# Kernel optimization log

Measured on AMD Instinct MI355X. Metric: run time of the kernel, lower is better.

The kernel has to match this reference:

```python
import jax, jax.numpy as jnp
import numpy as np

NU, NI, G, D, HD, OD = 8000, 10000, 4096, 64, 64, 64
ALPHA = 0.8      # self vs neighbor mixing in NodeApplyModule
EPS = 1e-8       # cosine-similarity denominator epsilon
NEG_BIG = -1e38  # replacement for all -inf rows


def setup_inputs() -> dict:
    key = jax.random.key(0)
    ks = jax.random.split(key, 24)
    def lin(k, o, i):
        return (jax.random.normal(k, (o, i), jnp.float32) * 0.02)
    def bias(k, o):
        return (jax.random.normal(k, (o,), jnp.float32) * 0.02)
    inp = {}
    inp["H"] = jax.random.randint(ks[0], (NU + NI, G), 0, 2, jnp.int32)
    inp["feats_weight"] = jax.random.normal(ks[1], (NU + NI, D), jnp.float32) * 0.1
    inp["num_groups"] = G
    # user SelfAttention params
    inp["u_Wq"] = lin(ks[2], HD, D); inp["u_bq"] = bias(ks[3], HD)
    inp["u_Wk"] = lin(ks[4], HD, D); inp["u_bk"] = bias(ks[5], HD)
    inp["u_Wv"] = lin(ks[6], HD, D); inp["u_bv"] = bias(ks[7], HD)
    inp["u_Ws"] = lin(ks[8], 1, NU); inp["u_bs"] = bias(ks[9], 1)
    # item SelfAttention params
    inp["i_Wq"] = lin(ks[10], HD, D); inp["i_bq"] = bias(ks[11], HD)
    inp["i_Wk"] = lin(ks[12], HD, D); inp["i_bk"] = bias(ks[13], HD)
    inp["i_Wv"] = lin(ks[14], HD, D); inp["i_bv"] = bias(ks[15], HD)
    inp["i_Ws"] = lin(ks[16], 1, NI); inp["i_bs"] = bias(ks[17], 1)
    # WeightedGCN NodeApplyModule linear: in_feats = 2*HD -> out_feats = OD
    inp["g_W"] = lin(ks[18], OD, 2 * HD); inp["g_b"] = bias(ks[19], OD)
    return inp


def _self_attention(x, mask, num_groups, Wq, bq, Wk, bk, Wv, bv, Ws, bs):
    # x: [N, D] ; mask: [N, G]
    q = x @ Wq.T + bq            # [N, HD]
    k = x @ Wk.T + bk            # [N, HD]
    v = x @ Wv.T + bv            # [N, HD]
    s = (q @ k.T) @ Ws.T + bs    # [N, 1]  (Linear(num_elem,1) over q@k.T)
    scores = jnp.broadcast_to(s.reshape(1, -1), (num_groups, x.shape[0]))  # [G, N]
    maskT = (mask == 0).T        # [G, N]
    scores = jnp.where(maskT, -jnp.inf, scores)
    all_inf = jnp.all(scores == -jnp.inf, axis=1, keepdims=True)
    scores = jnp.where(all_inf, jnp.float32(NEG_BIG), scores)
    w = jax.nn.softmax(scores, axis=1)   # [G, N]
    return w @ v, w                      # [G, HD], [G, N]


def reference(H, feats_weight, num_groups,
              u_Wq, u_bq, u_Wk, u_bk, u_Wv, u_bv, u_Ws, u_bs,
              i_Wq, i_bq, i_Wk, i_bk, i_Wv, i_bv, i_Ws, i_bs,
              g_W, g_b):
    users_feats = feats_weight[:NU]
    items_feats = feats_weight[NU:]
    users_mask = H[:NU]
    items_mask = H[NU:]

    gf_u, w_u = _self_attention(users_feats, users_mask, num_groups,
                                u_Wq, u_bq, u_Wk, u_bk, u_Wv, u_bv, u_Ws, u_bs)
    gf_i, w_i = _self_attention(items_feats, items_mask, num_groups,
                                i_Wq, i_bq, i_Wk, i_bk, i_Wv, i_bv, i_Ws, i_bs)
    # NaN scrubbing (faithful to torch.where(isnan, 0, .))
    gf_i = jnp.where(jnp.isnan(gf_i), 0.0, gf_i)
    w_i = jnp.where(jnp.isnan(w_i), 0.0, w_i)

    group_weights = jnp.concatenate([w_u, w_i], axis=1)   # [G, NU+NI]
    group_feats = jnp.concatenate([gf_u, gf_i], axis=1)   # [G, 2*HD]

    # similarity graph (cosine similarity of group weight rows)
    wp = group_weights @ group_weights.T                  # [G, G]
    norms = jnp.sqrt(jnp.sum(group_weights * group_weights, axis=1))
    l2 = 1.0 / (norms[:, None] * norms[None, :] + EPS)
    A = wp * l2  # edge weight src->dst at A[src, dst]; zero WP entries contribute 0

    # weighted mean aggregation (DGL msg/reduce: sum(w*h)/sum(w) over in-edges)
    msg = A.T @ group_feats                 # [G, 2*HD]: sum_src A[src,dst]*h[src]
    deg = jnp.sum(A, axis=0)[:, None]       # [G, 1]:   sum_src A[src,dst]
    h_neigh = jnp.where(deg > 0, msg / jnp.where(deg > 0, deg, 1.0), 0.0)

    agg = ALPHA * group_feats + (1.0 - ALPHA) * h_neigh
    out = jax.nn.sigmoid(agg @ g_W.T + g_b)               # [G, OD]
    return out
```

## Files before the change

kernel.cpp:

```cpp
#include <hip/hip_runtime.h>
#include <hip/hip_bf16.h>
#include <cstdint>
#include <cstddef>

#define NU   8000
#define NI   10000
#define NTOT 18000
#define G    4096
#define KP2  18176
#define NSL  284
#define NSL128 142
#define KT8  142
#define UT8  63

typedef __attribute__((ext_vector_type(4))) float f32x4;

__device__ __forceinline__ float bfu(unsigned short u){
  return __uint_as_float(((unsigned)u)<<16);
}
__device__ __forceinline__ unsigned short f2b(float f){
  __hip_bfloat16 h = __float2bfloat16(f);
  return __builtin_bit_cast(unsigned short, h);
}
__device__ __forceinline__ unsigned char f2f8(float v){
  int p = __builtin_amdgcn_cvt_pk_fp8_f32(v, 0.f, 0, false);
  return (unsigned char)(p & 0xff);
}
template<int SEL>
__device__ __forceinline__ float f8tof(unsigned int w){
  return __builtin_amdgcn_cvt_f32_fp8((int)w, SEL);
}
__device__ __forceinline__ void async16(void* lds, const void* g){
  __builtin_amdgcn_global_load_lds((const __attribute__((address_space(1))) unsigned int*)g,
                                   (__attribute__((address_space(3))) unsigned int*)lds, 16, 0, 0);
}
__device__ __forceinline__ int slot2n(int s){
  return (s < 8064) ? (s < 8000 ? s : -1) : (s-64 < NTOT ? s-64 : -1);
}

__global__ __launch_bounds__(256) void k_proj(
    const float* __restrict__ feats,
    const float* uWq, const float* ubq, const float* uWk, const float* ubk,
    const float* uWv, const float* ubv, const float* uWs,
    const float* iWq, const float* ibq, const float* iWk, const float* ibk,
    const float* iWv, const float* ibv, const float* iWs,
    float* __restrict__ q, unsigned short* __restrict__ vrow, float* __restrict__ wsk)
{
  __shared__ unsigned short Wt[6*4096];
  __shared__ float bl[6*64];
  __shared__ float wacc[128];
  const float* mats[6]  = {uWq,uWk,uWv,iWq,iWk,iWv};
  const float* bias6[6] = {ubq,ubk,ubv,ibq,ibk,ibv};
  int t = threadIdx.x;
  for (int m=0;m<6;m++)
    for (int e=t; e<4096; e+=256){
      int dd = e>>6, jj = e&63;
      Wt[m*4096 + jj*64 + dd] = f2b(mats[m][e]);
    }
  for (int e=t; e<384; e+=256) bl[e] = bias6[e>>6][e&63];
  if (t<128) wacc[t]=0.f;
  __syncthreads();
  int wave=t>>6, lane=t&63;
  int gw = blockIdx.x*4+wave, nw = gridDim.x*4;
  float accU=0.f, accI=0.f;
  for (int n=gw; n<NTOT; n+=nw){
    int br = (n>=NU);
    const unsigned short* W = Wt + br*3*4096;
    const float* bb = bl + br*192;
    float x = feats[(size_t)n*64+lane];
    float qd=bb[lane], kd=bb[64+lane], vd=bb[128+lane];
    #pragma unroll 16
    for (int j=0;j<64;j++){
      float xj = __shfl(x, j, 64);
      qd += xj * bfu(W[       j*64+lane]);
      kd += xj * bfu(W[4096 + j*64+lane]);
      vd += xj * bfu(W[8192 + j*64+lane]);
    }
    q[(size_t)n*64+lane] = qd;
    vrow[(size_t)n*64+lane] = f2b(vd);
    float wsn = br ? iWs[n-NU] : uWs[n];
    if (br) accI += wsn*kd; else accU += wsn*kd;
  }
  atomicAdd(&wacc[lane], accU);
  atomicAdd(&wacc[64+lane], accI);
  __syncthreads();
  if (t<128) atomicAdd(&wsk[t], wacc[t]);
}

__global__ __launch_bounds__(256) void k_score(const float* __restrict__ q, const float* __restrict__ wsk,
    const float* ubs, const float* ibs, float* __restrict__ rfs, unsigned char* __restrict__ rbs)
{
  __shared__ float wl[128];
  int t=threadIdx.x;
  if (t<128) wl[t]=wsk[t];
  __syncthreads();
  int slot = blockIdx.x*256+t;
  if (slot>=KP2) return;
  int n = slot2n(slot);
  if (n<0){ rfs[slot]=0.f; rbs[slot]=0; return; }
  int br = (slot>=8064);
  const float* wk = wl + br*64;
  float s = br ? ibs[0] : ubs[0];
  const float* qr = q + (size_t)n*64;
  #pragma unroll
  for (int d=0;d<64;d++) s += qr[d]*wk[d];
  unsigned char b = f2f8(expf(s));
  rbs[slot] = b;
  rfs[slot] = f8tof<0>((unsigned int)b);
}

__global__ __launch_bounds__(256) void k_buildW(
    const int* __restrict__ H, const float* __restrict__ rfs, const unsigned char* __restrict__ rbs,
    unsigned char* __restrict__ W8, unsigned char* __restrict__ W8t,
    float* __restrict__ Zu, float* __restrict__ Zi,
    float* __restrict__ S2u, float* __restrict__ S2i)
{
  __shared__ unsigned char Tb[128*136];
  __shared__ float rl[128];
  __shared__ unsigned char rb[128];
  __shared__ float zp[8][128];
  __shared__ float sp[8][128];
  int t = threadIdx.x;
  int s0 = blockIdx.x*128;
  int g0 = blockIdx.y*128;
  int isItem = (s0 >= 8064);
  if (t < 128){
    int n = slot2n(s0+t);
    rl[t] = (n>=0) ? rfs[s0+t] : 0.f;
    rb[t] = (n>=0) ? rbs[s0+t] : (unsigned char)0;
  }
  __syncthreads();
  int rgrp = t>>5;
  int gq   = (t&31)*4;
  int cc   = gq>>4;
  int gi4  = gq&15;
  float za[4]={0.f,0.f,0.f,0.f}, sa[4]={0.f,0.f,0.f,0.f};
  #pragma unroll
  for (int i=0;i<16;i++){
    int row = i*8 + rgrp;
    int n = slot2n(s0+row);
    uchar4 pk; pk.x=0; pk.y=0; pk.z=0; pk.w=0;
    if (n >= 0){
      int4 hv = *(const int4*)(H + (size_t)n*G + g0 + gq);
      unsigned char rbv = rb[row];
      float rq = rl[row];
      if (hv.x){ pk.x=rbv; za[0]+=rq; sa[0]+=rq*rq; }
      if (hv.y){ pk.y=rbv; za[1]+=rq; sa[1]+=rq*rq; }
      if (hv.z){ pk.z=rbv; za[2]+=rq; sa[2]+=rq*rq; }
      if (hv.w){ pk.w=rbv; za[3]+=rq; sa[3]+=rq*rq; }
    }
    int scc = cc ^ ((row>>3)&7);
    *(uchar4*)(Tb + row*136 + (scc<<4) + gi4) = pk;
  }
  #pragma unroll
  for (int e=0;e<4;e++){ zp[rgrp][gq+e]=za[e]; sp[rgrp][gq+e]=sa[e]; }
  __syncthreads();
  #pragma unroll
  for (int p=0;p<4;p++){
    int row = p*32 + (t>>3);
    int c   = t&7;
    int scc = c ^ ((row>>3)&7);
    uint4 v = *(const uint4*)(Tb + row*136 + (scc<<4));
    *(uint4*)(W8t + (size_t)(s0+row)*G + g0 + (c<<4)) = v;
  }
  #pragma unroll
  for (int p=0;p<4;p++){
    int gl = p*32 + (t>>3);
    int sc = (t&7)*16;
    int gcc = gl>>4, gb = gl&15;
    __align__(16) unsigned char buf[16];
    #pragma unroll
    for (int j=0;j<16;j++){
      int row = sc+j;
      int scc = gcc ^ ((row>>3)&7);
      buf[j] = Tb[row*136 + (scc<<4) + gb];
    }
    *(uint4*)(W8 + (size_t)(g0+gl)*KP2 + s0 + sc) = *(uint4*)buf;
  }
  if (t < 128){
    float z=0.f, s2=0.f;
    #pragma unroll
    for (int j=0;j<8;j++){ z += zp[j][t]; s2 += sp[j][t]; }
    if (isItem){ atomicAdd(&Zi[g0+t], z); atomicAdd(&S2i[g0+t], s2); }
    else       { atomicAdd(&Zu[g0+t], z); atomicAdd(&S2u[g0+t], s2); }
  }
}

__global__ __launch_bounds__(256) void k_mid(
    const float* __restrict__ Zu, const float* __restrict__ Zi,
    const float* __restrict__ S2u, const float* __restrict__ S2i,
    float* __restrict__ Cu, float* __restrict__ Ci,
    float* __restrict__ cnu, float* __restrict__ cni, float* __restrict__ ninv,
    unsigned char* __restrict__ cn8u, unsigned char* __restrict__ cn8i,
    unsigned char* __restrict__ W8, unsigned char* __restrict__ W8t,
    const unsigned short* __restrict__ vrow, unsigned char* __restrict__ vt8)
{
  __shared__ unsigned short tile[64][65];
  int b = blockIdx.x;
  int t = threadIdx.x;
  if (b == 0){
    for (int g=t; g<G; g+=256){
      float zu=Zu[g], zi=Zi[g];
      int fu = !(zu>0.f), fi = !(zi>0.f);
      float cu = fu ? (1.f/(float)NU) : 1.f/zu;
      float ci = fi ? (1.f/(float)NI) : 1.f/zi;
      float nu  = fu ? (1.f/(float)NU) : S2u[g]*cu*cu;
      float ni_ = fi ? (1.f/(float)NI) : S2i[g]*ci*ci;
      float nv = rsqrtf(nu+ni_);
      Cu[g]=cu; Ci[g]=ci; ninv[g]=nv; cnu[g]=cu*nv; cni[g]=ci*nv;
      cn8u[g] = f2f8(cu*nv*64.f);
      cn8i[g] = f2f8(ci*nv*64.f);
      if (fu){ for (int k=0;k<NU;k++){ W8[(size_t)g*KP2+k]=0x38; W8t[(size_t)k*G+g]=0x38; } }
      if (fi){ for (int k=0;k<NI;k++){ W8[(size_t)g*KP2+8064+k]=0x38; W8t[(size_t)(8064+k)*G+g]=0x38; } }
    }
    return;
  }
  int s0 = (b-1)*64;
  int tc = t&63, tr = t>>6;
  #pragma unroll
  for (int i=0;i<16;i++){
    int row = tr+i*4;
    int n = slot2n(s0+row);
    tile[row][tc] = (n>=0) ? vrow[(size_t)n*64+tc] : (unsigned short)0;
  }
  __syncthreads();
  int dOff = (s0 >= 8064) ? 64 : 0;
  #pragma unroll
  for (int i=0;i<16;i++){
    int dd = tr+i*4;
    float v = bfu(tile[tc][dd]) * 16.f;
    vt8[(size_t)(dOff+dd)*KP2 + s0+tc] = f2f8(v);
  }
}

template<int MODE>
__global__ __launch_bounds__(256) void k_gemm(
    const unsigned char* __restrict__ A, const unsigned char* __restrict__ B,
    float* __restrict__ Cs, float* __restrict__ degsl,
    const unsigned char* __restrict__ u8,
    const unsigned char* __restrict__ cn8u, const unsigned char* __restrict__ cn8i,
    float* __restrict__ uslice,
    long ldA, long ldB, long ldc)
{
  __shared__ __align__(16) unsigned char As[2][128*128];
  __shared__ __align__(16) unsigned char Bs[2][128*128];
  int t=threadIdx.x, wave=t>>6, lane=t&63;
  int I=blockIdx.x, J=blockIdx.y, z=blockIdx.z;
  int kt0=0, ktn=0;
  if (MODE==0){ kt0 = z*18; ktn = min(18, KT8-kt0); }
  else if (MODE==1){ kt0 = z*16; ktn = 16; }
  else {
    if (z<4){ kt0 = z*16;            ktn = min(16, UT8-kt0); }
    else    { kt0 = UT8 + (z-4)*20;  ktn = min(20, KT8-kt0); }
  }
  f32x4 acc[4][4];
  #pragma unroll
  for (int mi=0;mi<4;mi++)
    #pragma unroll
    for (int ni=0;ni<4;ni++){
      acc[mi][ni][0]=0.f; acc[mi][ni][1]=0.f; acc[mi][ni][2]=0.f; acc[mi][ni][3]=0.f;
    }
  f32x4 accd[4];
  if (MODE==2){
    #pragma unroll
    for (int mi=0;mi<4;mi++){ accd[mi][0]=0.f; accd[mi][1]=0.f; accd[mi][2]=0.f; accd[mi][3]=0.f; }
  }
  f32x4 accu[4];
  if (MODE==1){
    #pragma unroll
    for (int ni=0;ni<4;ni++){ accu[ni][0]=0.f; accu[ni][1]=0.f; accu[ni][2]=0.f; accu[ni][3]=0.f; }
  }
  int l7 = lane&7, q4 = lane>>4, cl15 = lane&15;
  int rowOff = wave*8 + (lane>>3);
  int cchunk = (lane&7) ^ ((lane>>3)&7);
  long aRow0 = (MODE==1) ? ((J>=UT8)?128:0) : (long)I*128;
  const unsigned char* Abase = A + aRow0*ldA + (long)cchunk*16;
  const unsigned char* Bbase = B + (long)J*128*ldB + (long)cchunk*16;
  const unsigned char* cnrow = (MODE==1) ? ((J>=UT8) ? cn8i : cn8u) : nullptr;
  int mrow0 = (wave&1)*64, nrow0 = (wave>>1)*64;

  auto STAGE = [&](int buf, int kt){
    long k0 = (long)kt*128;
    #pragma unroll
    for (int rr=0; rr<4; rr++){
      async16(As[buf] + wave*1024 + rr*4096, Abase + (long)(rr*32 + rowOff)*ldA + k0);
      async16(Bs[buf] + wave*1024 + rr*4096, Bbase + (long)(rr*32 + rowOff)*ldB + k0);
    }
  };

  STAGE(0, kt0);
  __syncthreads();

  for (int kt=kt0; kt<kt0+ktn; ++kt){
    int cur = (kt - kt0) & 1;
    if (kt+1 < kt0+ktn) STAGE(cur^1, kt+1);
    const unsigned char* Ab = As[cur];
    const unsigned char* Bb = Bs[cur];
    #pragma unroll
    for (int kk=0; kk<4; kk++){
      int xoff = (((kk*2 + (q4>>1)) ^ l7) << 4) + ((q4&1)<<3);
      long af[4], bf[4];
      #pragma unroll
      for (int mi=0;mi<4;mi++)
        af[mi] = *(const long*)(Ab + (mrow0 + mi*16 + cl15)*128 + xoff);
      #pragma unroll
      for (int ni=0;ni<4;ni++)
        bf[ni] = *(const long*)(Bb + (nrow0 + ni*16 + cl15)*128 + xoff);
      #pragma unroll
      for (int mi=0;mi<4;mi++)
        #pragma unroll
        for (int ni=0;ni<4;ni++)
          acc[mi][ni] = __builtin_amdgcn_mfma_f32_16x16x32_fp8_fp8(af[mi], bf[ni], acc[mi][ni], 0,0,0);
      if (MODE==2){
        long bu = 0;
        if (cl15==0) bu = *(const long*)(u8 + (size_t)kt*128 + kk*32 + q4*8);
        #pragma unroll
        for (int mi=0;mi<4;mi++)
          accd[mi] = __builtin_amdgcn_mfma_f32_16x16x32_fp8_fp8(af[mi], bu, accd[mi], 0,0,0);
      }
      if (MODE==1){
        long au = 0;
        if (cl15==0) au = *(const long*)(cnrow + (size_t)kt*128 + kk*32 + q4*8);
        #pragma unroll
        for (int ni=0;ni<4;ni++)
          accu[ni] = __builtin_amdgcn_mfma_f32_16x16x32_fp8_fp8(au, bf[ni], accu[ni], 0,0,0);
      }
    }
    __syncthreads();
  }
  int cq = lane>>4, cl = lane&15;
  float* slice = (MODE==1) ? (Cs + (size_t)z*128*KP2) : (Cs + (size_t)z*G*128);
  #pragma unroll
  for (int mi=0;mi<4;mi++)
    #pragma unroll
    for (int ni=0;ni<4;ni++)
      #pragma unroll
      for (int rg=0;rg<4;rg++){
        int gi = (MODE==1 ? 0 : I*128) + mrow0 + mi*16 + cq*4 + rg;
        int hi = J*128 + nrow0 + ni*16 + cl;
        slice[(size_t)gi*ldc + hi] = acc[mi][ni][rg];
      }
  if (MODE==2 && (wave>>1)==0 && cl15==0){
    #pragma unroll
    for (int mi=0;mi<4;mi++)
      #pragma unroll
      for (int rg=0;rg<4;rg++){
        int gi = I*128 + mrow0 + mi*16 + cq*4 + rg;
        degsl[(size_t)z*G + gi] = accd[mi][rg];
      }
  }
  if (MODE==1 && (wave&1)==0 && q4==0){
    #pragma unroll
    for (int ni=0;ni<4;ni++){
      int si = J*128 + nrow0 + ni*16 + cl15;
      uslice[(size_t)z*KP2 + si] = accu[ni][0];
    }
  }
}

__global__ __launch_bounds__(256) void k_gfpost(const float* __restrict__ gfsl,
    const float* __restrict__ Cu, const float* __restrict__ Ci, const float* __restrict__ ninv,
    float* __restrict__ gf, unsigned char* __restrict__ gfsT2_8)
{
  __shared__ float tile[64][65];
  int g0 = blockIdx.x*64, d0 = blockIdx.y*64;
  int tc=threadIdx.x&63, tr=threadIdx.x>>6;
  const float* Cd = blockIdx.y ? Ci : Cu;
  #pragma unroll
  for (int i=0;i<16;i++){
    int rr=tr+i*4;
    size_t off = (size_t)(g0+rr)*128 + d0+tc;
    float s = 0.f;
    #pragma unroll
    for (int zz=0;zz<8;zz++) s += gfsl[(size_t)zz*G*128 + off];
    float gfv = s * Cd[g0+rr] * 0.0625f;
    gf[off] = gfv;
    tile[rr][tc] = gfv * ninv[g0+rr];
  }
  __syncthreads();
  #pragma unroll
  for (int i=0;i<16;i++){
    int dd=tr+i*4;
    float v = tile[tc][dd] * 64.f;
    int g = g0+tc;
    gfsT2_8[(size_t)(d0+dd)*G + g]     = f2f8(v*Cu[g]);
    gfsT2_8[(size_t)(128+d0+dd)*G + g] = f2f8(v*Ci[g]);
  }
}

__global__ __launch_bounds__(256) void k_red1(const float* __restrict__ tmpsl,
    unsigned char* __restrict__ tmpT8, const float* __restrict__ uslice, unsigned char* __restrict__ u8){
  int b = blockIdx.x, t = threadIdx.x;
  if (b >= 2272){
    int idx2 = (b-2272)*256 + t;
    if (idx2 < KP2/4){
      size_t off = (size_t)idx2*4;
      f32x4 s = *(const f32x4*)(uslice + off);
      f32x4 s2 = *(const f32x4*)(uslice + (size_t)KP2 + off);
      uchar4 pk;
      pk.x = f2f8((s[0]+s2[0])*0.015625f);
      pk.y = f2f8((s[1]+s2[1])*0.015625f);
      pk.z = f2f8((s[2]+s2[2])*0.015625f);
      pk.w = f2f8((s[3]+s2[3])*0.015625f);
      *(uchar4*)(u8 + off) = pk;
    }
    return;
  }
  int idx = b*256 + t;
  int d = idx / 4544;
  int n = (idx - d*4544)*4;
  size_t off = (size_t)d*KP2 + n;
  f32x4 a = *(const f32x4*)(tmpsl + off);
  f32x4 c = *(const f32x4*)(tmpsl + (size_t)128*KP2 + off);
  uchar4 pk;
  pk.x = f2f8(a[0]+c[0]); pk.y = f2f8(a[1]+c[1]); pk.z = f2f8(a[2]+c[2]); pk.w = f2f8(a[3]+c[3]);
  *(uchar4*)(tmpT8 + off) = pk;
}

__global__ __launch_bounds__(256) void k_red2(const float* __restrict__ msgsl,
    const float* __restrict__ cnu, const float* __restrict__ cni, float* __restrict__ msg){
  int idx = blockIdx.x*256 + threadIdx.x;
  int gi = idx>>5;
  int hc = (idx&31)*4;
  size_t off = (size_t)gi*128 + hc;
  f32x4 su = {0.f,0.f,0.f,0.f}, si = {0.f,0.f,0.f,0.f};
  #pragma unroll
  for (int z=0;z<4;z++){
    f32x4 v = *(const f32x4*)(msgsl + (size_t)z*G*128 + off);
    su[0]+=v[0]; su[1]+=v[1]; su[2]+=v[2]; su[3]+=v[3];
  }
  #pragma unroll
  for (int z=4;z<8;z++){
    f32x4 v = *(const f32x4*)(msgsl + (size_t)z*G*128 + off);
    si[0]+=v[0]; si[1]+=v[1]; si[2]+=v[2]; si[3]+=v[3];
  }
  float a = cnu[gi]*0.015625f, b = cni[gi]*0.015625f;
  f32x4 r = {su[0]*a+si[0]*b, su[1]*a+si[1]*b, su[2]*a+si[2]*b, su[3]*a+si[3]*b};
  *(f32x4*)(msg + off) = r;
}

__global__ __launch_bounds__(256) void k_final(const float* __restrict__ gf, const float* __restrict__ msg,
    const float* __restrict__ degsl, const float* __restrict__ cnu, const float* __restrict__ cni,
    const float* __restrict__ gW, const float* __restrict__ gb, float* __restrict__ out)
{
  __shared__ float Wl[64*129];
  __shared__ float aggL[4][128];
  __shared__ float gbL[64];
  __shared__ float degL[4];
  int t=threadIdx.x;
  for (int e=t; e<8192; e+=256){ int o=e>>7, dd=e&127; Wl[o*129+dd] = gW[e]; }
  if (t<64) gbL[t] = gb[t];
  int g0 = blockIdx.x*4;
  if (t<4){
    int g = g0+t;
    float su=0.f, si=0.f;
    #pragma unroll
    for (int z=0;z<4;z++) su += degsl[(size_t)z*G + g];
    #pragma unroll
    for (int z=4;z<8;z++) si += degsl[(size_t)z*G + g];
    degL[t] = cnu[g]*su + cni[g]*si;
  }
  __syncthreads();
  for (int e=t; e<512; e+=256){
    int gl=e>>7, dd=e&127; int g=g0+gl;
    float dv = degL[gl];
    float hn = dv>0.f ? msg[(size_t)g*128+dd]/dv : 0.f;
    aggL[gl][dd] = 0.8f*gf[(size_t)g*128+dd] + 0.2f*hn;
  }
  __syncthreads();
  int gl = t>>6, o = t&63;
  float s = gbL[o];
  #pragma unroll
  for (int dd=0; dd<128; dd++) s += aggL[gl][dd]*Wl[o*129+dd];
  out[(size_t)(g0+gl)*64 + o] = 1.f/(1.f+expf(-s));
}

extern "C" void kernel_launch(void* const* d_in, const int* in_sizes, int n_in,
                              void* d_out, int out_size, void* d_ws, size_t ws_size,
                              hipStream_t stream)
{
  (void)in_sizes; (void)n_in; (void)out_size; (void)ws_size;
  const int* H = (const int*)d_in[0];
  const float* feats = (const float*)d_in[1];
  const float* uWq=(const float*)d_in[3];
  const float* ubq=(const float*)d_in[4];
  const float* uWk=(const float*)d_in[5];
  const float* ubk=(const float*)d_in[6];
  const float* uWv=(const float*)d_in[7];
  const float* ubv=(const float*)d_in[8];
  const float* uWs=(const float*)d_in[9];
  const float* ubs=(const float*)d_in[10];
  const float* iWq=(const float*)d_in[11];
  const float* ibq=(const float*)d_in[12];
  const float* iWk=(const float*)d_in[13];
  const float* ibk=(const float*)d_in[14];
  const float* iWv=(const float*)d_in[15];
  const float* ibv=(const float*)d_in[16];
  const float* iWs=(const float*)d_in[17];
  const float* ibs=(const float*)d_in[18];
  const float* gW =(const float*)d_in[19];
  const float* gb =(const float*)d_in[20];
  float* out = (float*)d_out;

  char* p = (char*)d_ws;
  auto alloc=[&](size_t b)->void*{ void* r=(void*)p; p += (b+255)&~(size_t)255; return r; };
  char* zbase = p;
  float* wsk  = (float*)alloc(128*4);
  float* Zu   = (float*)alloc(G*4);
  float* Zi   = (float*)alloc(G*4);
  float* S2u  = (float*)alloc(G*4);
  float* S2i  = (float*)alloc(G*4);
  unsigned char* vt8 = (unsigned char*)alloc((size_t)128*KP2);
  size_t zlen = (size_t)(p - zbase);
  unsigned char* W8    = (unsigned char*)alloc((size_t)G*KP2);
  unsigned char* W8t   = (unsigned char*)alloc((size_t)KP2*G);
  unsigned char* tmpT8 = (unsigned char*)alloc((size_t)128*KP2);
  unsigned char* gfsT2_8=(unsigned char*)alloc((size_t)256*G);
  float* gfsl = (float*)alloc((size_t)8*G*128*4);
  float* msgsl= (float*)alloc((size_t)8*G*128*4);
  float* tmpsl= (float*)alloc((size_t)2*128*KP2*4);
  float* uslice=(float*)alloc((size_t)2*KP2*4);
  float* degsl= (float*)alloc((size_t)8*G*4);
  float* gf   = (float*)alloc((size_t)G*128*4);
  float* msg  = (float*)alloc((size_t)G*128*4);
  float* q    = (float*)alloc((size_t)NTOT*64*4);
  unsigned short* vrow=(unsigned short*)alloc((size_t)NTOT*64*2);
  float* rfs  = (float*)alloc((size_t)KP2*4);
  unsigned char* rbs = (unsigned char*)alloc((size_t)KP2);
  float* Cu   = (float*)alloc(G*4);
  float* Ci   = (float*)alloc(G*4);
  float* cnu  = (float*)alloc(G*4);
  float* cni  = (float*)alloc(G*4);
  float* ninv = (float*)alloc(G*4);
  unsigned char* cn8u = (unsigned char*)alloc(G);
  unsigned char* cn8i = (unsigned char*)alloc(G);
  unsigned char* u8 = (unsigned char*)alloc((size_t)KP2);

  (void)hipMemsetAsync(zbase, 0, zlen, stream);

  k_proj<<<256,256,0,stream>>>(feats, uWq,ubq,uWk,ubk,uWv,ubv,uWs,
                               iWq,ibq,iWk,ibk,iWv,ibv,iWs, q, vrow, wsk);
  k_score<<<(KP2+255)/256,256,0,stream>>>(q, wsk, ubs, ibs, rfs, rbs);
  k_buildW<<<dim3(NSL128,32),256,0,stream>>>(H, rfs, rbs, W8, W8t, Zu, Zi, S2u, S2i);
  k_mid<<<NSL+1,256,0,stream>>>(Zu,Zi,S2u,S2i,Cu,Ci,cnu,cni,ninv,cn8u,cn8i,W8,W8t,vrow,vt8);
  k_gemm<0><<<dim3(32,1,8),256,0,stream>>>(W8, vt8, gfsl, nullptr, nullptr, nullptr, nullptr, nullptr,
                                           (long)KP2, (long)KP2, 128);
  k_gfpost<<<dim3(64,2),256,0,stream>>>(gfsl, Cu, Ci, ninv, gf, gfsT2_8);
  k_gemm<1><<<dim3(1,KT8,2),256,0,stream>>>(gfsT2_8, W8t, tmpsl, nullptr, nullptr, cn8u, cn8i, uslice,
                                            (long)G, (long)G, (long)KP2);
  k_red1<<<2272+18,256,0,stream>>>(tmpsl, tmpT8, uslice, u8);
  k_gemm<2><<<dim3(32,1,8),256,0,stream>>>(W8, tmpT8, msgsl, degsl, u8, nullptr, nullptr, nullptr,
                                           (long)KP2, (long)KP2, 128);
  k_red2<<<512,256,0,stream>>>(msgsl, cnu, cni, msg);
  k_final<<<G/4,256,0,stream>>>(gf, msg, degsl, cnu, cni, gW, gb, out);
}
```

Before: 708.7 us.

## Double split-K slices across GEMMs and use wave-per-row reduction in score kernel

Doubles the split-K factor for all three fp8 GEMM stages (16 z-slices for the G-dimension GEMMs, 4 for the transposed one), which puts more workgroups on the GPU, and updates the reduction kernels to sum the extra partial slices. The separate partial-sum buffers are merged into one reused workspace. k_score now gives each slot a full wave: the dot product is spread across the lanes and reduced with shuffles, replacing the serial per-thread loop. The added cost is more partial-sum traffic and reduction work in exchange for better occupancy of the main GEMMs.

```diff
diff --git a/kernel.cpp b/kernel.cpp
--- a/kernel.cpp
+++ b/kernel.cpp
@@ -91,22 +91,31 @@
     const float* ubs, const float* ibs, float* __restrict__ rfs, unsigned char* __restrict__ rbs)
 {
   __shared__ float wl[128];
+  __shared__ float bs2[2];
   int t=threadIdx.x;
   if (t<128) wl[t]=wsk[t];
-  __syncthreads();
-  int slot = blockIdx.x*256+t;
-  if (slot>=KP2) return;
-  int n = slot2n(slot);
-  if (n<0){ rfs[slot]=0.f; rbs[slot]=0; return; }
-  int br = (slot>=8064);
-  const float* wk = wl + br*64;
-  float s = br ? ibs[0] : ubs[0];
-  const float* qr = q + (size_t)n*64;
-  #pragma unroll
-  for (int d=0;d<64;d++) s += qr[d]*wk[d];
-  unsigned char b = f2f8(expf(s));
-  rbs[slot] = b;
-  rfs[slot] = f8tof<0>((unsigned int)b);
+  if (t==128) bs2[0]=ubs[0];
+  if (t==129) bs2[1]=ibs[0];
+  __syncthreads();
+  int wave=t>>6, lane=t&63;
+  #pragma unroll 4
+  for (int i=0;i<32;i++){
+    int slot = blockIdx.x*128 + i*4 + wave;
+    int n = slot2n(slot);
+    int br = (slot>=8064);
+    float v = 0.f;
+    if (n>=0) v = q[(size_t)n*64+lane] * wl[br*64+lane];
+    #pragma unroll
+    for (int m=32;m>=1;m>>=1) v += __shfl_xor(v, m, 64);
+    if (lane==0){
+      if (n>=0){
+        unsigned char b = f2f8(expf(v + bs2[br]));
+        rbs[slot]=b; rfs[slot]=f8tof<0>((unsigned int)b);
+      } else {
+        rbs[slot]=0; rfs[slot]=0.f;
+      }
+    }
+  }
 }
 
 __global__ __launch_bounds__(256) void k_buildW(
@@ -247,11 +256,11 @@
   int t=threadIdx.x, wave=t>>6, lane=t&63;
   int I=blockIdx.x, J=blockIdx.y, z=blockIdx.z;
   int kt0=0, ktn=0;
-  if (MODE==0){ kt0 = z*18; ktn = min(18, KT8-kt0); }
-  else if (MODE==1){ kt0 = z*16; ktn = 16; }
+  if (MODE==0){ kt0 = z*9; ktn = min(9, KT8-kt0); }
+  else if (MODE==1){ kt0 = z*8; ktn = 8; }
   else {
-    if (z<4){ kt0 = z*16;            ktn = min(16, UT8-kt0); }
-    else    { kt0 = UT8 + (z-4)*20;  ktn = min(20, KT8-kt0); }
+    if (z<8){ kt0 = z*8;             ktn = min(8, UT8-kt0); }
+    else    { kt0 = UT8 + (z-8)*10;  ktn = min(10, KT8-kt0); }
   }
   f32x4 acc[4][4];
   #pragma unroll
@@ -372,7 +381,7 @@
     size_t off = (size_t)(g0+rr)*128 + d0+tc;
     float s = 0.f;
     #pragma unroll
-    for (int zz=0;zz<8;zz++) s += gfsl[(size_t)zz*G*128 + off];
+    for (int zz=0;zz<16;zz++) s += gfsl[(size_t)zz*G*128 + off];
     float gfv = s * Cd[g0+rr] * 0.0625f;
     gf[off] = gfv;
     tile[rr][tc] = gfv * ninv[g0+rr];
@@ -396,12 +405,16 @@
     if (idx2 < KP2/4){
       size_t off = (size_t)idx2*4;
       f32x4 s = *(const f32x4*)(uslice + off);
-      f32x4 s2 = *(const f32x4*)(uslice + (size_t)KP2 + off);
+      #pragma unroll
+      for (int z=1;z<4;z++){
+        f32x4 v = *(const f32x4*)(uslice + (size_t)z*KP2 + off);
+        s[0]+=v[0]; s[1]+=v[1]; s[2]+=v[2]; s[3]+=v[3];
+      }
       uchar4 pk;
-      pk.x = f2f8((s[0]+s2[0])*0.015625f);
-      pk.y = f2f8((s[1]+s2[1])*0.015625f);
-      pk.z = f2f8((s[2]+s2[2])*0.015625f);
-      pk.w = f2f8((s[3]+s2[3])*0.015625f);
+      pk.x = f2f8(s[0]*0.015625f);
+      pk.y = f2f8(s[1]*0.015625f);
+      pk.z = f2f8(s[2]*0.015625f);
+      pk.w = f2f8(s[3]*0.015625f);
       *(uchar4*)(u8 + off) = pk;
     }
     return;
@@ -410,10 +423,14 @@
   int d = idx / 4544;
   int n = (idx - d*4544)*4;
   size_t off = (size_t)d*KP2 + n;
-  f32x4 a = *(const f32x4*)(tmpsl + off);
-  f32x4 c = *(const f32x4*)(tmpsl + (size_t)128*KP2 + off);
+  f32x4 s = *(const f32x4*)(tmpsl + off);
+  #pragma unroll
+  for (int z=1;z<4;z++){
+    f32x4 v = *(const f32x4*)(tmpsl + (size_t)z*128*KP2 + off);
+    s[0]+=v[0]; s[1]+=v[1]; s[2]+=v[2]; s[3]+=v[3];
+  }
   uchar4 pk;
-  pk.x = f2f8(a[0]+c[0]); pk.y = f2f8(a[1]+c[1]); pk.z = f2f8(a[2]+c[2]); pk.w = f2f8(a[3]+c[3]);
+  pk.x = f2f8(s[0]); pk.y = f2f8(s[1]); pk.z = f2f8(s[2]); pk.w = f2f8(s[3]);
   *(uchar4*)(tmpT8 + off) = pk;
 }
 
@@ -425,12 +442,12 @@
   size_t off = (size_t)gi*128 + hc;
   f32x4 su = {0.f,0.f,0.f,0.f}, si = {0.f,0.f,0.f,0.f};
   #pragma unroll
-  for (int z=0;z<4;z++){
+  for (int z=0;z<8;z++){
     f32x4 v = *(const f32x4*)(msgsl + (size_t)z*G*128 + off);
     su[0]+=v[0]; su[1]+=v[1]; su[2]+=v[2]; su[3]+=v[3];
   }
   #pragma unroll
-  for (int z=4;z<8;z++){
+  for (int z=8;z<16;z++){
     f32x4 v = *(const f32x4*)(msgsl + (size_t)z*G*128 + off);
     si[0]+=v[0]; si[1]+=v[1]; si[2]+=v[2]; si[3]+=v[3];
   }
@@ -455,9 +472,9 @@
     int g = g0+t;
     float su=0.f, si=0.f;
     #pragma unroll
-    for (int z=0;z<4;z++) su += degsl[(size_t)z*G + g];
-    #pragma unroll
-    for (int z=4;z<8;z++) si += degsl[(size_t)z*G + g];
+    for (int z=0;z<8;z++) su += degsl[(size_t)z*G + g];
+    #pragma unroll
+    for (int z=8;z<16;z++) si += degsl[(size_t)z*G + g];
     degL[t] = cnu[g]*su + cni[g]*si;
   }
   __syncthreads();
@@ -516,11 +533,9 @@
   unsigned char* W8t   = (unsigned char*)alloc((size_t)KP2*G);
   unsigned char* tmpT8 = (unsigned char*)alloc((size_t)128*KP2);
   unsigned char* gfsT2_8=(unsigned char*)alloc((size_t)256*G);
-  float* gfsl = (float*)alloc((size_t)8*G*128*4);
-  float* msgsl= (float*)alloc((size_t)8*G*128*4);
-  float* tmpsl= (float*)alloc((size_t)2*128*KP2*4);
-  float* uslice=(float*)alloc((size_t)2*KP2*4);
-  float* degsl= (float*)alloc((size_t)8*G*4);
+  float* slb  = (float*)alloc((size_t)4*128*KP2*4);
+  float* uslice=(float*)alloc((size_t)4*KP2*4);
+  float* degsl= (float*)alloc((size_t)16*G*4);
   float* gf   = (float*)alloc((size_t)G*128*4);
   float* msg  = (float*)alloc((size_t)G*128*4);
   float* q    = (float*)alloc((size_t)NTOT*64*4);
@@ -540,17 +555,17 @@
 
   k_proj<<<256,256,0,stream>>>(feats, uWq,ubq,uWk,ubk,uWv,ubv,uWs,
                                iWq,ibq,iWk,ibk,iWv,ibv,iWs, q, vrow, wsk);
-  k_score<<<(KP2+255)/256,256,0,stream>>>(q, wsk, ubs, ibs, rfs, rbs);
+  k_score<<<KP2/128,256,0,stream>>>(q, wsk, ubs, ibs, rfs, rbs);
   k_buildW<<<dim3(NSL128,32),256,0,stream>>>(H, rfs, rbs, W8, W8t, Zu, Zi, S2u, S2i);
   k_mid<<<NSL+1,256,0,stream>>>(Zu,Zi,S2u,S2i,Cu,Ci,cnu,cni,ninv,cn8u,cn8i,W8,W8t,vrow,vt8);
-  k_gemm<0><<<dim3(32,1,8),256,0,stream>>>(W8, vt8, gfsl, nullptr, nullptr, nullptr, nullptr, nullptr,
+  k_gemm<0><<<dim3(32,1,16),256,0,stream>>>(W8, vt8, slb, nullptr, nullptr, nullptr, nullptr, nullptr,
                                            (long)KP2, (long)KP2, 128);
-  k_gfpost<<<dim3(64,2),256,0,stream>>>(gfsl, Cu, Ci, ninv, gf, gfsT2_8);
-  k_gemm<1><<<dim3(1,KT8,2),256,0,stream>>>(gfsT2_8, W8t, tmpsl, nullptr, nullptr, cn8u, cn8i, uslice,
+  k_gfpost<<<dim3(64,2),256,0,stream>>>(slb, Cu, Ci, ninv, gf, gfsT2_8);
+  k_gemm<1><<<dim3(1,KT8,4),256,0,stream>>>(gfsT2_8, W8t, slb, nullptr, nullptr, cn8u, cn8i, uslice,
                                             (long)G, (long)G, (long)KP2);
-  k_red1<<<2272+18,256,0,stream>>>(tmpsl, tmpT8, uslice, u8);
-  k_gemm<2><<<dim3(32,1,8),256,0,stream>>>(W8, tmpT8, msgsl, degsl, u8, nullptr, nullptr, nullptr,
+  k_red1<<<2272+18,256,0,stream>>>(slb, tmpT8, uslice, u8);
+  k_gemm<2><<<dim3(32,1,16),256,0,stream>>>(W8, tmpT8, slb, degsl, u8, nullptr, nullptr, nullptr,
                                            (long)KP2, (long)KP2, 128);
-  k_red2<<<512,256,0,stream>>>(msgsl, cnu, cni, msg);
+  k_red2<<<512,256,0,stream>>>(slb, cnu, cni, msg);
   k_final<<<G/4,256,0,stream>>>(gf, msg, degsl, cnu, cni, gW, gb, out);
 }
```

Measured after the change: 700.9 us. Within noise of the previous version (-1.1%).
